# Optimization experiments

Hardware: AMD Instinct MI355X
Metric: run time of the kernel (lower is better)

Reference implementation:

```python
import jax, jax.numpy as jnp
import numpy as np

B, C, H_RES, W_RES = 8, 192, 64, 64


def dwconv(x, kern, pad):
    # depthwise conv, x: (B,C,H,W), kern: (C,1,k,k)
    return jax.lax.conv_general_dilated(
        x, kern, window_strides=(1, 1), padding=[(pad, pad), (pad, pad)],
        dimension_numbers=('NCHW', 'OIHW', 'NCHW'),
        feature_group_count=x.shape[1])


def omni_shift(x, alpha, dw1, dw3, dw5):
    # OmniShift (training branch): learnable mix of identity + depthwise 1x1/3x3/5x5
    return (alpha[0] * x + alpha[1] * dwconv(x, dw1, 0)
            + alpha[2] * dwconv(x, dw3, 1) + alpha[3] * dwconv(x, dw5, 2))


def biwkv(w, u, k, v):
    # Bidirectional WKV (Vision-RWKV style):
    # out_t = (sum_{i!=t} e^{-(|t-i|-1)w + k_i} v_i + e^{u+k_t} v_t)
    #       / (sum_{i!=t} e^{-(|t-i|-1)w + k_i}       + e^{u+k_t})
    # w,u: (C,); k,v: (B,T,C). Implemented as two stable log-scaled scans.
    kT = jnp.moveaxis(k, 1, 0)  # (T,B,C)
    vT = jnp.moveaxis(v, 1, 0)
    bc = (k.shape[0], k.shape[2])
    init = (jnp.full(bc, -jnp.inf, k.dtype), jnp.zeros(bc, k.dtype), jnp.zeros(bc, k.dtype))

    def step(carry, inp):
        p, num, den = carry          # state = e^p * (num, den) over strictly-previous tokens
        kt, vt = inp
        out = (p, num, den)          # emit BEFORE absorbing token t (i != t term)
        q = jnp.maximum(p - w, kt)
        e1 = jnp.exp(p - w - q)
        e2 = jnp.exp(kt - q)
        return (q, e1 * num + e2 * vt, e1 * den + e2), out

    _, (pf, nf, df) = jax.lax.scan(step, init, (kT, vT))
    _, (pb, nb, db) = jax.lax.scan(step, init, (kT[::-1], vT[::-1]))
    pb, nb, db = pb[::-1], nb[::-1], db[::-1]

    ps = u + kT                      # self term exponent
    r = jnp.maximum(jnp.maximum(pf, pb), ps)
    ef, eb, es = jnp.exp(pf - r), jnp.exp(pb - r), jnp.exp(ps - r)
    out = (ef * nf + eb * nb + es * vT) / (ef * df + eb * db + es)
    return jnp.moveaxis(out, 0, 1)   # (B,T,C)


def setup_inputs() -> dict:
    key = jax.random.key(0)
    ks = jax.random.split(key, 12)
    s = 1.0 / np.sqrt(C)
    inp = {
        'x': jax.random.normal(ks[0], (B, C, H_RES, W_RES), jnp.float32),
        'w_key': jax.random.normal(ks[1], (C, C), jnp.float32) * s,
        'w_value': jax.random.normal(ks[2], (C, C), jnp.float32) * s,
        'w_recept': jax.random.normal(ks[3], (C, C), jnp.float32) * s,
        'w_out': jax.random.normal(ks[4], (C, C), jnp.float32) * s,
        'decay': jax.random.normal(ks[5], (C,), jnp.float32),
        'boost': jax.random.normal(ks[6], (C,), jnp.float32),
        'alpha': jax.random.normal(ks[7], (4,), jnp.float32),
        'dw1': jax.random.normal(ks[8], (C, 1, 1, 1), jnp.float32) * s,
        'dw3': jax.random.normal(ks[9], (C, 1, 3, 3), jnp.float32) * (s / 3.0),
        'dw5': jax.random.normal(ks[10], (C, 1, 5, 5), jnp.float32) * (s / 5.0),
        'H': H_RES,
        'W': W_RES,
    }
    return inp


def reference(x, w_key, w_value, w_recept, w_out, decay, boost, alpha, dw1, dw3, dw5, H, W):
    Bn, Cn = x.shape[0], x.shape[1]
    T = H * W
    xs = omni_shift(x, alpha, dw1, dw3, dw5)                 # (B,C,H,W)
    xt = jnp.transpose(xs.reshape(Bn, Cn, T), (0, 2, 1))     # (B,T,C)
    k = jnp.einsum('btc,dc->btd', xt, w_key)
    v = jnp.einsum('btc,dc->btd', xt, w_value)
    sr = jax.nn.sigmoid(jnp.einsum('btc,dc->btd', xt, w_recept))
    y = biwkv(decay / T, boost / T, k, v)                    # (B,T,C)
    y = sr * y
    y = jnp.einsum('btd,cd->btc', y, w_out)
    return jnp.transpose(y, (0, 2, 1)).reshape(Bn, Cn, H, W)
```

## Files before the change

kernel.cpp:

```cpp
#include <hip/hip_runtime.h>
#include <math.h>

#define Cn 192
#define Bn 8
#define Tn 4096
#define HW 64

typedef unsigned short u16;
typedef unsigned int u32;
typedef __attribute__((ext_vector_type(8))) __bf16 bf16x8;
typedef __attribute__((ext_vector_type(16))) float f32x16;

__device__ __forceinline__ void gload16(const void* g, void* l) {
    __builtin_amdgcn_global_load_lds(
        (const __attribute__((address_space(1))) void*)g,
        (__attribute__((address_space(3))) void*)l, 16, 0, 0);
}

__device__ __forceinline__ void split_bf16(float x, u16 &h, u16 &l) {
    u32 u = __float_as_uint(x);
    u32 uh = (u + 0x7FFFu + ((u >> 16) & 1u)) & 0xFFFF0000u;
    h = (u16)(uh >> 16);
    float r = x - __uint_as_float(uh);
    u32 ur = __float_as_uint(r);
    l = (u16)((ur + 0x7FFFu + ((ur >> 16) & 1u)) >> 16);
}

__global__ __launch_bounds__(256) void omni_kernel(const float* __restrict__ x,
                                                   const float* __restrict__ alpha,
                                                   const float* __restrict__ dw1,
                                                   const float* __restrict__ dw3,
                                                   const float* __restrict__ dw5,
                                                   u16* __restrict__ xhi,
                                                   u16* __restrict__ xlo) {
    const int plane = blockIdx.x;
    const int c = plane % Cn;
    const float* xin = x + (size_t)plane * Tn;
    u16* oh = xhi + (size_t)plane * Tn;
    u16* ol = xlo + (size_t)plane * Tn;

    __shared__ float tile[68 * 68];
    __shared__ float wk[25];

    const int tid = threadIdx.x;
    if (tid == 0) {
        const float a0 = alpha[0], a1 = alpha[1], a2 = alpha[2], a3 = alpha[3];
        #pragma unroll
        for (int j = 0; j < 25; ++j) wk[j] = a3 * dw5[c * 25 + j];
        #pragma unroll
        for (int dy = 0; dy < 3; ++dy)
            #pragma unroll
            for (int dx = 0; dx < 3; ++dx)
                wk[(dy + 1) * 5 + (dx + 1)] += a2 * dw3[c * 9 + dy * 3 + dx];
        wk[12] += a1 * dw1[c] + a0;
    }
    for (int i = tid; i < 68 * 68; i += 256) {
        int r = i / 68, cc = i - r * 68;
        int gy = r - 2, gx = cc - 2;
        float v = 0.f;
        if (gy >= 0 && gy < HW && gx >= 0 && gx < HW) v = xin[gy * HW + gx];
        tile[i] = v;
    }
    __syncthreads();

    const int py = tid >> 3;
    const int px0 = (tid & 7) << 3;

    #pragma unroll
    for (int half = 0; half < 2; ++half) {
        const int y = py + half * 32;
        float row[5][12];
        #pragma unroll
        for (int dy = 0; dy < 5; ++dy) {
            const float4* rp = (const float4*)&tile[(y + dy) * 68 + px0];
            float4 r0 = rp[0], r1 = rp[1], r2 = rp[2];
            row[dy][0] = r0.x; row[dy][1] = r0.y; row[dy][2]  = r0.z; row[dy][3]  = r0.w;
            row[dy][4] = r1.x; row[dy][5] = r1.y; row[dy][6]  = r1.z; row[dy][7]  = r1.w;
            row[dy][8] = r2.x; row[dy][9] = r2.y; row[dy][10] = r2.z; row[dy][11] = r2.w;
        }
        u32 ph[4], pl[4];
        #pragma unroll
        for (int jj = 0; jj < 8; ++jj) {
            float acc = 0.f;
            #pragma unroll
            for (int dy = 0; dy < 5; ++dy)
                #pragma unroll
                for (int dx = 0; dx < 5; ++dx)
                    acc = fmaf(row[dy][jj + dx], wk[dy * 5 + dx], acc);
            u16 h, l2;
            split_bf16(acc, h, l2);
            if (jj & 1) { ph[jj >> 1] |= ((u32)h) << 16; pl[jj >> 1] |= ((u32)l2) << 16; }
            else        { ph[jj >> 1] = h;               pl[jj >> 1] = l2; }
        }
        *(uint4*)&oh[y * 64 + px0] = make_uint4(ph[0], ph[1], ph[2], ph[3]);
        *(uint4*)&ol[y * 64 + px0] = make_uint4(pl[0], pl[1], pl[2], pl[3]);
    }
}

__global__ __launch_bounds__(256) void transpose_kernel(const u16* __restrict__ ih,
                                                        const u16* __restrict__ il,
                                                        u16* __restrict__ oh,
                                                        u16* __restrict__ ol,
                                                        const float* __restrict__ Wk,
                                                        const float* __restrict__ Wv,
                                                        const float* __restrict__ Wr,
                                                        const float* __restrict__ Wo,
                                                        u16* __restrict__ wh,
                                                        u16* __restrict__ wl) {
    const int tid = threadIdx.x;
    if (blockIdx.z == 8) {
        const int base = (blockIdx.y * 32 + blockIdx.x) * 768;
        #pragma unroll
        for (int j = 0; j < 3; ++j) {
            int idx = base + j * 256 + tid;
            int mat = idx / 36864;
            int off = idx - mat * 36864;
            const float* src = (mat == 0) ? Wk : (mat == 1) ? Wv : (mat == 2) ? Wr : Wo;
            u16 h, l;
            split_bf16(src[off], h, l);
            wh[idx] = h;
            wl[idx] = l;
        }
        return;
    }

    __shared__ u32 T[2][128][21];
    const size_t ib = (size_t)blockIdx.z * Cn * Tn;
    const int c0 = blockIdx.y * 32, t0 = blockIdx.x * 128;

    {
        const int c2 = tid >> 4;
        const int tc = (tid & 15) * 8;
        const size_t ge = ib + (size_t)(c0 + 2 * c2) * Tn + t0 + tc;
        uint4 evh = *(const uint4*)&ih[ge];
        uint4 odh = *(const uint4*)&ih[ge + Tn];
        uint4 evl = *(const uint4*)&il[ge];
        uint4 odl = *(const uint4*)&il[ge + Tn];
        const u32 eh4[4] = {evh.x, evh.y, evh.z, evh.w};
        const u32 oh4[4] = {odh.x, odh.y, odh.z, odh.w};
        const u32 el4[4] = {evl.x, evl.y, evl.z, evl.w};
        const u32 ol4[4] = {odl.x, odl.y, odl.z, odl.w};
        #pragma unroll
        for (int q = 0; q < 4; ++q) {
            T[0][tc + 2 * q    ][c2] = (eh4[q] & 0xFFFFu) | (oh4[q] << 16);
            T[0][tc + 2 * q + 1][c2] = (eh4[q] >> 16) | (oh4[q] & 0xFFFF0000u);
            T[1][tc + 2 * q    ][c2] = (el4[q] & 0xFFFFu) | (ol4[q] << 16);
            T[1][tc + 2 * q + 1][c2] = (el4[q] >> 16) | (ol4[q] & 0xFFFF0000u);
        }
    }
    __syncthreads();
    {
        const int t = tid >> 1;
        const int hf = tid & 1;
        u32 wv[8][2];
        #pragma unroll
        for (int q = 0; q < 8; ++q) {
            wv[q][0] = T[0][t][hf * 8 + q];
            wv[q][1] = T[1][t][hf * 8 + q];
        }
        const size_t go = ib + (size_t)(t0 + t) * Cn + c0 + hf * 16;
        *(uint4*)&oh[go]     = make_uint4(wv[0][0], wv[1][0], wv[2][0], wv[3][0]);
        *(uint4*)&oh[go + 8] = make_uint4(wv[4][0], wv[5][0], wv[6][0], wv[7][0]);
        *(uint4*)&ol[go]     = make_uint4(wv[0][1], wv[1][1], wv[2][1], wv[3][1]);
        *(uint4*)&ol[go + 8] = make_uint4(wv[4][1], wv[5][1], wv[6][1], wv[7][1]);
    }
}

template<int NM>
__global__ __launch_bounds__(256) void gemm_mfma(const u16* __restrict__ wh,
                                                 const u16* __restrict__ wl,
                                                 const u16* __restrict__ Xh,
                                                 const u16* __restrict__ Xl,
                                                 float* __restrict__ O0,
                                                 float* __restrict__ O1,
                                                 float* __restrict__ O2,
                                                 int wrow0) {
    constexpr int ASZ = NM * 64 * 32;
    constexpr int BSZ = 128 * 32;
    __shared__ u16 A_[2 * ASZ];
    __shared__ u16 B_[2][2 * BSZ];

    const int tid  = threadIdx.x;
    const int l    = tid & 63;
    const int wave = tid >> 6;
    const int wm   = wave >> 1, wn = wave & 1;
    const int m0   = blockIdx.y * 64;
    const int t0   = blockIdx.x * 128;
    const size_t xb = (size_t)blockIdx.z * Cn * Tn;

    f32x16 acc[NM][2];
    #pragma unroll
    for (int m = 0; m < NM; ++m)
        #pragma unroll
        for (int nf = 0; nf < 2; ++nf)
            #pragma unroll
            for (int r = 0; r < 16; ++r) acc[m][nf][r] = 0.f;

    auto stageA = [&](int k0) {
        #pragma unroll
        for (int i = 0; i < NM; ++i) {
            int idx = i * 256 + tid;
            int row = idx >> 2;
            int cb  = (idx & 3) ^ ((row >> 1) & 3);
            int grow = wrow0 + (row >> 6) * 192 + m0 + (row & 63);
            int dst = (i * 256 + wave * 64) * 8;
            gload16(wh + (size_t)grow * Cn + k0 + cb * 8, A_ + dst);
            gload16(wl + (size_t)grow * Cn + k0 + cb * 8, A_ + ASZ + dst);
        }
    };
    auto stageB = [&](int bf, int k0) {
        #pragma unroll
        for (int i = 0; i < 2; ++i) {
            int idx = i * 256 + tid;
            int tr  = idx >> 2;
            int cb  = (idx & 3) ^ ((tr >> 1) & 3);
            int dst = (i * 256 + wave * 64) * 8;
            gload16(Xh + xb + (size_t)(t0 + tr) * Cn + k0 + cb * 8, B_[bf] + dst);
            gload16(Xl + xb + (size_t)(t0 + tr) * Cn + k0 + cb * 8, B_[bf] + BSZ + dst);
        }
    };
    auto compute = [&](int bf) {
        const u16* Ah = A_;
        const u16* Al = A_ + ASZ;
        const u16* Bh = B_[bf];
        const u16* Bl = B_[bf] + BSZ;
        #pragma unroll
        for (int kh = 0; kh < 2; ++kh) {
            const int cbb = kh * 2 + (l >> 5);
            bf16x8 ah[NM], al[NM];
            #pragma unroll
            for (int m = 0; m < NM; ++m) {
                int r = m * 64 + wm * 32 + (l & 31);
                int off = r * 32 + ((cbb ^ ((r >> 1) & 3)) << 3);
                ah[m] = *(const bf16x8*)&Ah[off];
                al[m] = *(const bf16x8*)&Al[off];
            }
            #pragma unroll
            for (int nf = 0; nf < 2; ++nf) {
                int tr = wn * 64 + nf * 32 + (l & 31);
                int off = tr * 32 + ((cbb ^ ((tr >> 1) & 3)) << 3);
                bf16x8 bh = *(const bf16x8*)&Bh[off];
                bf16x8 bl = *(const bf16x8*)&Bl[off];
                #pragma unroll
                for (int m = 0; m < NM; ++m) {
                    acc[m][nf] = __builtin_amdgcn_mfma_f32_32x32x16_bf16(ah[m], bh, acc[m][nf], 0, 0, 0);
                    acc[m][nf] = __builtin_amdgcn_mfma_f32_32x32x16_bf16(ah[m], bl, acc[m][nf], 0, 0, 0);
                    acc[m][nf] = __builtin_amdgcn_mfma_f32_32x32x16_bf16(al[m], bh, acc[m][nf], 0, 0, 0);
                }
            }
        }
    };

    stageA(0);
    stageB(0, 0);
    __syncthreads();
    for (int ks = 0; ks < 6; ++ks) {
        if (ks < 5) stageB((ks + 1) & 1, (ks + 1) * 32);
        compute(ks & 1);
        __syncthreads();
        if (ks < 5) {
            stageA((ks + 1) * 32);
            __syncthreads();
        }
    }

    float* Os[3] = {O0, O1, O2};
    #pragma unroll
    for (int m = 0; m < NM; ++m) {
        float* O = Os[m] + (size_t)blockIdx.z * Cn * Tn;
        #pragma unroll
        for (int nf = 0; nf < 2; ++nf) {
            int col = t0 + wn * 64 + nf * 32 + (l & 31);
            #pragma unroll
            for (int r = 0; r < 16; ++r) {
                int row = m0 + wm * 32 + (r & 3) + 8 * (r >> 2) + 4 * (l >> 5);
                O[(size_t)row * Tn + col] = acc[m][nf][r];
            }
        }
    }
}

__global__ __launch_bounds__(256) void wkv_kernel(const float* __restrict__ kg,
                                                  const float* __restrict__ vg,
                                                  const float* __restrict__ srlg,
                                                  const float* __restrict__ decay,
                                                  const float* __restrict__ boost,
                                                  u16* __restrict__ yhi,
                                                  u16* __restrict__ ylo) {
    const int row = blockIdx.x;
    const int d = row % Cn;
    const float* kr = kg + (size_t)row * Tn;
    const float* vr = vg + (size_t)row * Tn;
    const float* sr = srlg + (size_t)row * Tn;
    u16* yh = yhi + (size_t)row * Tn;
    u16* yl = ylo + (size_t)row * Tn;

    const int tid = threadIdx.x;
    const int t0 = tid * 16;

    float kk[16], vv[16];
    #pragma unroll
    for (int j = 0; j < 16; j += 4) {
        *(float4*)&kk[j] = *(const float4*)&kr[t0 + j];
        *(float4*)&vv[j] = *(const float4*)&vr[t0 + j];
    }

    __shared__ float red[256];
    float lm = kk[0];
    #pragma unroll
    for (int j = 1; j < 16; ++j) lm = fmaxf(lm, kk[j]);
    red[tid] = lm;
    __syncthreads();
    for (int s = 128; s > 0; s >>= 1) {
        if (tid < s) red[tid] = fmaxf(red[tid], red[tid + s]);
        __syncthreads();
    }
    const float m = red[0];
    __syncthreads();

    const float ww = decay[d] * (1.0f / (float)Tn);
    const float u = boost[d] * (1.0f / (float)Tn);
    const float lam = expf(-ww);
    const float lam16 = expf(-16.0f * ww);

    float a[16];
    #pragma unroll
    for (int j = 0; j < 16; ++j) a[j] = expf(kk[j] - m);

    float SN = 0.f, SD = 0.f;
    #pragma unroll
    for (int j = 0; j < 16; ++j) { SN = fmaf(lam, SN, a[j] * vv[j]); SD = fmaf(lam, SD, a[j]); }
    float BN = 0.f, BD = 0.f;
    #pragma unroll
    for (int j = 15; j >= 0; --j) { BN = fmaf(lam, BN, a[j] * vv[j]); BD = fmaf(lam, BD, a[j]); }

    __shared__ float sN[2][256], sD[2][256];

    sN[0][tid] = SN; sD[0][tid] = SD;
    __syncthreads();
    int src = 0;
    float f = lam16;
    for (int o = 1; o < 256; o <<= 1) {
        float nN = sN[src][tid], nD = sD[src][tid];
        if (tid >= o) { nN = fmaf(f, sN[src][tid - o], nN); nD = fmaf(f, sD[src][tid - o], nD); }
        sN[src ^ 1][tid] = nN; sD[src ^ 1][tid] = nD;
        __syncthreads();
        src ^= 1; f = f * f;
    }
    const float CfN = (tid > 0) ? sN[src][tid - 1] : 0.f;
    const float CfD = (tid > 0) ? sD[src][tid - 1] : 0.f;
    __syncthreads();

    sN[0][tid] = BN; sD[0][tid] = BD;
    __syncthreads();
    src = 0; f = lam16;
    for (int o = 1; o < 256; o <<= 1) {
        float nN = sN[src][tid], nD = sD[src][tid];
        if (tid + o < 256) { nN = fmaf(f, sN[src][tid + o], nN); nD = fmaf(f, sD[src][tid + o], nD); }
        sN[src ^ 1][tid] = nN; sD[src ^ 1][tid] = nD;
        __syncthreads();
        src ^= 1; f = f * f;
    }
    const float CbN = (tid < 255) ? sN[src][tid + 1] : 0.f;
    const float CbD = (tid < 255) ? sD[src][tid + 1] : 0.f;

    float fN[16], fD[16];
    float cN = CfN, cD = CfD;
    #pragma unroll
    for (int j = 0; j < 16; ++j) {
        fN[j] = cN; fD[j] = cD;
        cN = fmaf(lam, cN, a[j] * vv[j]);
        cD = fmaf(lam, cD, a[j]);
    }

    float sl[16];
    #pragma unroll
    for (int j = 0; j < 16; j += 4) *(float4*)&sl[j] = *(const float4*)&sr[t0 + j];

    u16 oh[16], ol[16];
    float bN = CbN, bD = CbD;
    #pragma unroll
    for (int j = 15; j >= 0; --j) {
        const float es = expf(u + kk[j] - m);
        const float num = fN[j] + bN + es * vv[j];
        const float den = fD[j] + bD + es;
        const float y = num / den;
        const float sig = 1.0f / (1.0f + expf(-sl[j]));
        split_bf16(sig * y, oh[j], ol[j]);
        bN = fmaf(lam, bN, a[j] * vv[j]);
        bD = fmaf(lam, bD, a[j]);
    }

    u32 ph[8], pl[8];
    #pragma unroll
    for (int j = 0; j < 8; ++j) {
        ph[j] = (u32)oh[2 * j] | ((u32)oh[2 * j + 1] << 16);
        pl[j] = (u32)ol[2 * j] | ((u32)ol[2 * j + 1] << 16);
    }
    *(uint4*)&yh[t0]     = make_uint4(ph[0], ph[1], ph[2], ph[3]);
    *(uint4*)&yh[t0 + 8] = make_uint4(ph[4], ph[5], ph[6], ph[7]);
    *(uint4*)&yl[t0]     = make_uint4(pl[0], pl[1], pl[2], pl[3]);
    *(uint4*)&yl[t0 + 8] = make_uint4(pl[4], pl[5], pl[6], pl[7]);
}

extern "C" void kernel_launch(void* const* d_in, const int* in_sizes, int n_in,
                              void* d_out, int out_size, void* d_ws, size_t ws_size,
                              hipStream_t stream) {
    const float* x        = (const float*)d_in[0];
    const float* w_key    = (const float*)d_in[1];
    const float* w_value  = (const float*)d_in[2];
    const float* w_recept = (const float*)d_in[3];
    const float* w_out    = (const float*)d_in[4];
    const float* decay    = (const float*)d_in[5];
    const float* boost    = (const float*)d_in[6];
    const float* alpha    = (const float*)d_in[7];
    const float* dw1      = (const float*)d_in[8];
    const float* dw3      = (const float*)d_in[9];
    const float* dw5      = (const float*)d_in[10];

    const size_t S = (size_t)Bn * Cn * Tn;
    u16* R0 = (u16*)d_ws;
    u16* R1 = R0 + 2 * S;
    u16* R2 = R1 + 2 * S;
    u16* whp = R2 + 2 * S;
    u16* wlp = whp + 4 * 36864;

    u16* xs_hi = R0;        u16* xs_lo = R0 + S;
    u16* Xt_hi = R1;        u16* Xt_lo = R1 + S;
    float* kb  = (float*)R0;
    float* vb  = (float*)R2;
    float* srl = (float*)d_out;
    u16* y_hi  = R1;        u16* y_lo  = R1 + S;
    u16* Yt_hi = R2;        u16* Yt_lo = R2 + S;
    float* out = (float*)d_out;

    omni_kernel<<<dim3(Bn * Cn), 256, 0, stream>>>(x, alpha, dw1, dw3, dw5, xs_hi, xs_lo);

    transpose_kernel<<<dim3(32, 6, 9), 256, 0, stream>>>(xs_hi, xs_lo, Xt_hi, Xt_lo,
                                                         w_key, w_value, w_recept, w_out,
                                                         whp, wlp);

    gemm_mfma<3><<<dim3(32, 3, 8), 256, 0, stream>>>(whp, wlp, Xt_hi, Xt_lo, kb, vb, srl, 0);

    wkv_kernel<<<dim3(Bn * Cn), 256, 0, stream>>>(kb, vb, srl, decay, boost, y_hi, y_lo);

    transpose_kernel<<<dim3(32, 6, 8), 256, 0, stream>>>(y_hi, y_lo, Yt_hi, Yt_lo,
                                                         w_key, w_value, w_recept, w_out,
                                                         whp, wlp);

    gemm_mfma<1><<<dim3(32, 3, 8), 256, 0, stream>>>(whp, wlp, Yt_hi, Yt_lo, out, nullptr, nullptr, 576);
}
```

Baseline: 119.2 us.

## Fuse transposes into GEMM B-loads and weight split into omni kernel

Removes both standalone transpose kernels. The GEMM now reads the channel-major bf16 hi/lo activations directly, transposes 4x4 u16 quads in registers with lane shuffles, and writes them into a padded, swizzled LDS buffer. A-operand weights are loaded straight from global memory into registers instead of being staged through LDS. The weight hi/lo split moves into extra blocks of the omni kernel, cutting two launches and the full activation round-trips through memory. In exchange it adds shuffle work and register pressure, plus a hand-managed barrier/prefetch pipeline with s_setprio.

Result: slower. 143.2 us (+20.2%).

```diff
diff --git a/kernel.cpp b/kernel.cpp
--- a/kernel.cpp
+++ b/kernel.cpp
@@ -10,12 +10,6 @@
 typedef unsigned int u32;
 typedef __attribute__((ext_vector_type(8))) __bf16 bf16x8;
 typedef __attribute__((ext_vector_type(16))) float f32x16;
-
-__device__ __forceinline__ void gload16(const void* g, void* l) {
-    __builtin_amdgcn_global_load_lds(
-        (const __attribute__((address_space(1))) void*)g,
-        (__attribute__((address_space(3))) void*)l, 16, 0, 0);
-}
 
 __device__ __forceinline__ void split_bf16(float x, u16 &h, u16 &l) {
     u32 u = __float_as_uint(x);
@@ -31,8 +25,31 @@
                                                    const float* __restrict__ dw1,
                                                    const float* __restrict__ dw3,
                                                    const float* __restrict__ dw5,
+                                                   const float* __restrict__ Wk,
+                                                   const float* __restrict__ Wv,
+                                                   const float* __restrict__ Wr,
+                                                   const float* __restrict__ Wo,
                                                    u16* __restrict__ xhi,
-                                                   u16* __restrict__ xlo) {
+                                                   u16* __restrict__ xlo,
+                                                   u16* __restrict__ wh,
+                                                   u16* __restrict__ wl) {
+    const int tid = threadIdx.x;
+    if (blockIdx.x >= 1536) {
+        const int base = (blockIdx.x - 1536) * 768;
+        #pragma unroll
+        for (int jj = 0; jj < 3; ++jj) {
+            int idx = base + jj * 256 + tid;
+            int mat = idx / 36864;
+            int off = idx - mat * 36864;
+            const float* src = (mat == 0) ? Wk : (mat == 1) ? Wv : (mat == 2) ? Wr : Wo;
+            u16 h, l;
+            split_bf16(src[off], h, l);
+            wh[idx] = h;
+            wl[idx] = l;
+        }
+        return;
+    }
+
     const int plane = blockIdx.x;
     const int c = plane % Cn;
     const float* xin = x + (size_t)plane * Tn;
@@ -42,7 +59,6 @@
     __shared__ float tile[68 * 68];
     __shared__ float wk[25];
 
-    const int tid = threadIdx.x;
     if (tid == 0) {
         const float a0 = alpha[0], a1 = alpha[1], a2 = alpha[2], a3 = alpha[3];
         #pragma unroll
@@ -97,88 +113,35 @@
     }
 }
 
-__global__ __launch_bounds__(256) void transpose_kernel(const u16* __restrict__ ih,
-                                                        const u16* __restrict__ il,
-                                                        u16* __restrict__ oh,
-                                                        u16* __restrict__ ol,
-                                                        const float* __restrict__ Wk,
-                                                        const float* __restrict__ Wv,
-                                                        const float* __restrict__ Wr,
-                                                        const float* __restrict__ Wo,
-                                                        u16* __restrict__ wh,
-                                                        u16* __restrict__ wl) {
-    const int tid = threadIdx.x;
-    if (blockIdx.z == 8) {
-        const int base = (blockIdx.y * 32 + blockIdx.x) * 768;
-        #pragma unroll
-        for (int j = 0; j < 3; ++j) {
-            int idx = base + j * 256 + tid;
-            int mat = idx / 36864;
-            int off = idx - mat * 36864;
-            const float* src = (mat == 0) ? Wk : (mat == 1) ? Wv : (mat == 2) ? Wr : Wo;
-            u16 h, l;
-            split_bf16(src[off], h, l);
-            wh[idx] = h;
-            wl[idx] = l;
-        }
-        return;
-    }
-
-    __shared__ u32 T[2][128][21];
-    const size_t ib = (size_t)blockIdx.z * Cn * Tn;
-    const int c0 = blockIdx.y * 32, t0 = blockIdx.x * 128;
-
-    {
-        const int c2 = tid >> 4;
-        const int tc = (tid & 15) * 8;
-        const size_t ge = ib + (size_t)(c0 + 2 * c2) * Tn + t0 + tc;
-        uint4 evh = *(const uint4*)&ih[ge];
-        uint4 odh = *(const uint4*)&ih[ge + Tn];
-        uint4 evl = *(const uint4*)&il[ge];
-        uint4 odl = *(const uint4*)&il[ge + Tn];
-        const u32 eh4[4] = {evh.x, evh.y, evh.z, evh.w};
-        const u32 oh4[4] = {odh.x, odh.y, odh.z, odh.w};
-        const u32 el4[4] = {evl.x, evl.y, evl.z, evl.w};
-        const u32 ol4[4] = {odl.x, odl.y, odl.z, odl.w};
-        #pragma unroll
-        for (int q = 0; q < 4; ++q) {
-            T[0][tc + 2 * q    ][c2] = (eh4[q] & 0xFFFFu) | (oh4[q] << 16);
-            T[0][tc + 2 * q + 1][c2] = (eh4[q] >> 16) | (oh4[q] & 0xFFFF0000u);
-            T[1][tc + 2 * q    ][c2] = (el4[q] & 0xFFFFu) | (ol4[q] << 16);
-            T[1][tc + 2 * q + 1][c2] = (el4[q] >> 16) | (ol4[q] & 0xFFFF0000u);
-        }
-    }
-    __syncthreads();
-    {
-        const int t = tid >> 1;
-        const int hf = tid & 1;
-        u32 wv[8][2];
-        #pragma unroll
-        for (int q = 0; q < 8; ++q) {
-            wv[q][0] = T[0][t][hf * 8 + q];
-            wv[q][1] = T[1][t][hf * 8 + q];
-        }
-        const size_t go = ib + (size_t)(t0 + t) * Cn + c0 + hf * 16;
-        *(uint4*)&oh[go]     = make_uint4(wv[0][0], wv[1][0], wv[2][0], wv[3][0]);
-        *(uint4*)&oh[go + 8] = make_uint4(wv[4][0], wv[5][0], wv[6][0], wv[7][0]);
-        *(uint4*)&ol[go]     = make_uint4(wv[0][1], wv[1][1], wv[2][1], wv[3][1]);
-        *(uint4*)&ol[go + 8] = make_uint4(wv[4][1], wv[5][1], wv[6][1], wv[7][1]);
-    }
+__device__ __forceinline__ uint2 quad_transpose(uint2 v, int j) {
+    unsigned int p0 = (unsigned int)__shfl_xor((int)v.x, 1);
+    unsigned int p1 = (unsigned int)__shfl_xor((int)v.y, 1);
+    unsigned int g0, g1;
+    if ((j & 1) == 0) {
+        g0 = (p0 << 16) | (v.x & 0xFFFFu);
+        g1 = (p1 << 16) | (v.y & 0xFFFFu);
+    } else {
+        g0 = (v.x & 0xFFFF0000u) | (p0 >> 16);
+        g1 = (v.y & 0xFFFF0000u) | (p1 >> 16);
+    }
+    unsigned int s0 = (unsigned int)__shfl_xor((int)g0, 2);
+    unsigned int s1 = (unsigned int)__shfl_xor((int)g1, 2);
+    uint2 f;
+    if ((j & 2) == 0) { f.x = g0; f.y = s0; }
+    else              { f.x = s1; f.y = g1; }
+    return f;
 }
 
 template<int NM>
-__global__ __launch_bounds__(256) void gemm_mfma(const u16* __restrict__ wh,
-                                                 const u16* __restrict__ wl,
-                                                 const u16* __restrict__ Xh,
-                                                 const u16* __restrict__ Xl,
-                                                 float* __restrict__ O0,
-                                                 float* __restrict__ O1,
-                                                 float* __restrict__ O2,
-                                                 int wrow0) {
-    constexpr int ASZ = NM * 64 * 32;
-    constexpr int BSZ = 128 * 32;
-    __shared__ u16 A_[2 * ASZ];
-    __shared__ u16 B_[2][2 * BSZ];
+__global__ __launch_bounds__(256) void gemm_fused(const u16* __restrict__ wh,
+                                                  const u16* __restrict__ wl,
+                                                  const u16* __restrict__ Xh,
+                                                  const u16* __restrict__ Xl,
+                                                  float* __restrict__ O0,
+                                                  float* __restrict__ O1,
+                                                  float* __restrict__ O2,
+                                                  int wrow0) {
+    __shared__ u16 B_[2][2][128 * 40];
 
     const int tid  = threadIdx.x;
     const int l    = tid & 63;
@@ -187,6 +150,7 @@
     const int m0   = blockIdx.y * 64;
     const int t0   = blockIdx.x * 128;
     const size_t xb = (size_t)blockIdx.z * Cn * Tn;
+    const int j    = tid & 3;
 
     f32x16 acc[NM][2];
     #pragma unroll
@@ -196,71 +160,89 @@
             #pragma unroll
             for (int r = 0; r < 16; ++r) acc[m][nf][r] = 0.f;
 
-    auto stageA = [&](int k0) {
-        #pragma unroll
-        for (int i = 0; i < NM; ++i) {
-            int idx = i * 256 + tid;
-            int row = idx >> 2;
-            int cb  = (idx & 3) ^ ((row >> 1) & 3);
-            int grow = wrow0 + (row >> 6) * 192 + m0 + (row & 63);
-            int dst = (i * 256 + wave * 64) * 8;
-            gload16(wh + (size_t)grow * Cn + k0 + cb * 8, A_ + dst);
-            gload16(wl + (size_t)grow * Cn + k0 + cb * 8, A_ + ASZ + dst);
+    uint2 rbh[4], rbl[4];
+    bf16x8 rah[NM][2], ral[NM][2];
+
+    auto loadB = [&](int k0) {
+        #pragma unroll
+        for (int p = 0; p < 4; ++p) {
+            int cq = 2 * p + (wave >> 1);
+            int tq = ((wave & 1) << 4) + (l >> 2);
+            size_t g = xb + (size_t)(k0 + cq * 4 + j) * Tn + t0 + tq * 4;
+            rbh[p] = *(const uint2*)&Xh[g];
+            rbl[p] = *(const uint2*)&Xl[g];
         }
     };
-    auto stageB = [&](int bf, int k0) {
-        #pragma unroll
-        for (int i = 0; i < 2; ++i) {
-            int idx = i * 256 + tid;
-            int tr  = idx >> 2;
-            int cb  = (idx & 3) ^ ((tr >> 1) & 3);
-            int dst = (i * 256 + wave * 64) * 8;
-            gload16(Xh + xb + (size_t)(t0 + tr) * Cn + k0 + cb * 8, B_[bf] + dst);
-            gload16(Xl + xb + (size_t)(t0 + tr) * Cn + k0 + cb * 8, B_[bf] + BSZ + dst);
-        }
+    auto writeB = [&](int bf) {
+        u16* Bh = &B_[bf][0][0];
+        u16* Bl = &B_[bf][1][0];
+        #pragma unroll
+        for (int p = 0; p < 4; ++p) {
+            int cq = 2 * p + (wave >> 1);
+            int tq = ((wave & 1) << 4) + (l >> 2);
+            uint2 th = quad_transpose(rbh[p], j);
+            uint2 tl = quad_transpose(rbl[p], j);
+            int t = tq * 4 + j;
+            int blk = ((cq >> 1) ^ (t >> 1) ^ (t >> 3)) & 3;
+            int off = t * 40 + (blk << 3) + ((cq & 1) << 2);
+            *(uint2*)&Bh[off] = th;
+            *(uint2*)&Bl[off] = tl;
+        }
+    };
+    auto loadA = [&](int k0) {
+        #pragma unroll
+        for (int m = 0; m < NM; ++m)
+            #pragma unroll
+            for (int kh = 0; kh < 2; ++kh) {
+                int cbb = kh * 2 + (l >> 5);
+                int r = wrow0 + m * 192 + m0 + wm * 32 + (l & 31);
+                size_t g = (size_t)r * Cn + k0 + cbb * 8;
+                rah[m][kh] = *(const bf16x8*)&wh[g];
+                ral[m][kh] = *(const bf16x8*)&wl[g];
+            }
     };
     auto compute = [&](int bf) {
-        const u16* Ah = A_;
-        const u16* Al = A_ + ASZ;
-        const u16* Bh = B_[bf];
-        const u16* Bl = B_[bf] + BSZ;
+        const u16* Bh = &B_[bf][0][0];
+        const u16* Bl = &B_[bf][1][0];
         #pragma unroll
         for (int kh = 0; kh < 2; ++kh) {
             const int cbb = kh * 2 + (l >> 5);
-            bf16x8 ah[NM], al[NM];
-            #pragma unroll
-            for (int m = 0; m < NM; ++m) {
-                int r = m * 64 + wm * 32 + (l & 31);
-                int off = r * 32 + ((cbb ^ ((r >> 1) & 3)) << 3);
-                ah[m] = *(const bf16x8*)&Ah[off];
-                al[m] = *(const bf16x8*)&Al[off];
-            }
             #pragma unroll
             for (int nf = 0; nf < 2; ++nf) {
-                int tr = wn * 64 + nf * 32 + (l & 31);
-                int off = tr * 32 + ((cbb ^ ((tr >> 1) & 3)) << 3);
+                int t = wn * 64 + nf * 32 + (l & 31);
+                int off = t * 40 + (((cbb ^ (t >> 1) ^ (t >> 3)) & 3) << 3);
                 bf16x8 bh = *(const bf16x8*)&Bh[off];
                 bf16x8 bl = *(const bf16x8*)&Bl[off];
                 #pragma unroll
                 for (int m = 0; m < NM; ++m) {
-                    acc[m][nf] = __builtin_amdgcn_mfma_f32_32x32x16_bf16(ah[m], bh, acc[m][nf], 0, 0, 0);
-                    acc[m][nf] = __builtin_amdgcn_mfma_f32_32x32x16_bf16(ah[m], bl, acc[m][nf], 0, 0, 0);
-                    acc[m][nf] = __builtin_amdgcn_mfma_f32_32x32x16_bf16(al[m], bh, acc[m][nf], 0, 0, 0);
+                    acc[m][nf] = __builtin_amdgcn_mfma_f32_32x32x16_bf16(rah[m][kh], bh, acc[m][nf], 0, 0, 0);
+                    acc[m][nf] = __builtin_amdgcn_mfma_f32_32x32x16_bf16(rah[m][kh], bl, acc[m][nf], 0, 0, 0);
+                    acc[m][nf] = __builtin_amdgcn_mfma_f32_32x32x16_bf16(ral[m][kh], bh, acc[m][nf], 0, 0, 0);
                 }
             }
         }
     };
 
-    stageA(0);
-    stageB(0, 0);
-    __syncthreads();
+    loadB(0);
+    loadA(0);
+    writeB(0);
+    loadB(32);
+    asm volatile("s_waitcnt lgkmcnt(0)" ::: "memory");
+    __builtin_amdgcn_sched_barrier(0);
+    __builtin_amdgcn_s_barrier();
+
+    #pragma unroll
     for (int ks = 0; ks < 6; ++ks) {
-        if (ks < 5) stageB((ks + 1) & 1, (ks + 1) * 32);
+        __builtin_amdgcn_s_setprio(1);
         compute(ks & 1);
-        __syncthreads();
+        __builtin_amdgcn_s_setprio(0);
         if (ks < 5) {
-            stageA((ks + 1) * 32);
-            __syncthreads();
+            writeB((ks + 1) & 1);
+            asm volatile("s_waitcnt lgkmcnt(0)" ::: "memory");
+            __builtin_amdgcn_sched_barrier(0);
+            __builtin_amdgcn_s_barrier();
+            if (ks < 4) loadB((ks + 2) * 32);
+            loadA((ks + 1) * 32);
         }
     }
 
@@ -426,27 +408,19 @@
     u16* wlp = whp + 4 * 36864;
 
     u16* xs_hi = R0;        u16* xs_lo = R0 + S;
-    u16* Xt_hi = R1;        u16* Xt_lo = R1 + S;
-    float* kb  = (float*)R0;
+    float* kb  = (float*)R1;
     float* vb  = (float*)R2;
     float* srl = (float*)d_out;
-    u16* y_hi  = R1;        u16* y_lo  = R1 + S;
-    u16* Yt_hi = R2;        u16* Yt_lo = R2 + S;
+    u16* y_hi  = R0;        u16* y_lo  = R0 + S;
     float* out = (float*)d_out;
 
-    omni_kernel<<<dim3(Bn * Cn), 256, 0, stream>>>(x, alpha, dw1, dw3, dw5, xs_hi, xs_lo);
-
-    transpose_kernel<<<dim3(32, 6, 9), 256, 0, stream>>>(xs_hi, xs_lo, Xt_hi, Xt_lo,
-                                                         w_key, w_value, w_recept, w_out,
-                                                         whp, wlp);
-
-    gemm_mfma<3><<<dim3(32, 3, 8), 256, 0, stream>>>(whp, wlp, Xt_hi, Xt_lo, kb, vb, srl, 0);
+    omni_kernel<<<dim3(1536 + 192), 256, 0, stream>>>(x, alpha, dw1, dw3, dw5,
+                                                      w_key, w_value, w_recept, w_out,
+                                                      xs_hi, xs_lo, whp, wlp);
+
+    gemm_fused<3><<<dim3(32, 3, 8), 256, 0, stream>>>(whp, wlp, xs_hi, xs_lo, kb, vb, srl, 0);
 
     wkv_kernel<<<dim3(Bn * Cn), 256, 0, stream>>>(kb, vb, srl, decay, boost, y_hi, y_lo);
 
-    transpose_kernel<<<dim3(32, 6, 8), 256, 0, stream>>>(y_hi, y_lo, Yt_hi, Yt_lo,
-                                                         w_key, w_value, w_recept, w_out,
-                                                         whp, wlp);
-
-    gemm_mfma<1><<<dim3(32, 3, 8), 256, 0, stream>>>(whp, wlp, Yt_hi, Yt_lo, out, nullptr, nullptr, 576);
-}
+    gemm_fused<1><<<dim3(32, 3, 8), 256, 0, stream>>>(whp, wlp, y_hi, y_lo, out, nullptr, nullptr, 576);
+}
```

## Single-buffer GEMM staging and move weight splitting into omni kernel

Applied to the files above, without the earlier changes.

Replaces the double-buffered B tile staging in the MFMA GEMM with a single shared buffer for A and B, loaded together with syncs on both sides of the load. This cuts LDS use per block, which may allow more resident blocks per CU, but load/compute overlap inside a block is lost. The fp32-to-bf16 hi/lo weight splitting moves from an extra z-slice of the first transpose launch into extra blocks of the omni convolution kernel, which simplifies the transpose kernel.

Measured after the change: 121.9 us. 1.02x slower.

```diff
diff --git a/kernel.cpp b/kernel.cpp
--- a/kernel.cpp
+++ b/kernel.cpp
@@ -31,8 +31,31 @@
                                                    const float* __restrict__ dw1,
                                                    const float* __restrict__ dw3,
                                                    const float* __restrict__ dw5,
+                                                   const float* __restrict__ Wk,
+                                                   const float* __restrict__ Wv,
+                                                   const float* __restrict__ Wr,
+                                                   const float* __restrict__ Wo,
                                                    u16* __restrict__ xhi,
-                                                   u16* __restrict__ xlo) {
+                                                   u16* __restrict__ xlo,
+                                                   u16* __restrict__ wh,
+                                                   u16* __restrict__ wl) {
+    const int tid = threadIdx.x;
+    if (blockIdx.x >= 1536) {
+        const int base = (blockIdx.x - 1536) * 768;
+        #pragma unroll
+        for (int jj = 0; jj < 3; ++jj) {
+            int idx = base + jj * 256 + tid;
+            int mat = idx / 36864;
+            int off = idx - mat * 36864;
+            const float* src = (mat == 0) ? Wk : (mat == 1) ? Wv : (mat == 2) ? Wr : Wo;
+            u16 h, l;
+            split_bf16(src[off], h, l);
+            wh[idx] = h;
+            wl[idx] = l;
+        }
+        return;
+    }
+
     const int plane = blockIdx.x;
     const int c = plane % Cn;
     const float* xin = x + (size_t)plane * Tn;
@@ -42,7 +65,6 @@
     __shared__ float tile[68 * 68];
     __shared__ float wk[25];
 
-    const int tid = threadIdx.x;
     if (tid == 0) {
         const float a0 = alpha[0], a1 = alpha[1], a2 = alpha[2], a3 = alpha[3];
         #pragma unroll
@@ -100,31 +122,9 @@
 __global__ __launch_bounds__(256) void transpose_kernel(const u16* __restrict__ ih,
                                                         const u16* __restrict__ il,
                                                         u16* __restrict__ oh,
-                                                        u16* __restrict__ ol,
-                                                        const float* __restrict__ Wk,
-                                                        const float* __restrict__ Wv,
-                                                        const float* __restrict__ Wr,
-                                                        const float* __restrict__ Wo,
-                                                        u16* __restrict__ wh,
-                                                        u16* __restrict__ wl) {
+                                                        u16* __restrict__ ol) {
+    __shared__ u32 T[2][128][21];
     const int tid = threadIdx.x;
-    if (blockIdx.z == 8) {
-        const int base = (blockIdx.y * 32 + blockIdx.x) * 768;
-        #pragma unroll
-        for (int j = 0; j < 3; ++j) {
-            int idx = base + j * 256 + tid;
-            int mat = idx / 36864;
-            int off = idx - mat * 36864;
-            const float* src = (mat == 0) ? Wk : (mat == 1) ? Wv : (mat == 2) ? Wr : Wo;
-            u16 h, l;
-            split_bf16(src[off], h, l);
-            wh[idx] = h;
-            wl[idx] = l;
-        }
-        return;
-    }
-
-    __shared__ u32 T[2][128][21];
     const size_t ib = (size_t)blockIdx.z * Cn * Tn;
     const int c0 = blockIdx.y * 32, t0 = blockIdx.x * 128;
 
@@ -177,8 +177,8 @@
                                                  int wrow0) {
     constexpr int ASZ = NM * 64 * 32;
     constexpr int BSZ = 128 * 32;
-    __shared__ u16 A_[2 * ASZ];
-    __shared__ u16 B_[2][2 * BSZ];
+    __shared__ u16 Ah_[ASZ], Al_[ASZ];
+    __shared__ u16 Bh_[BSZ], Bl_[BSZ];
 
     const int tid  = threadIdx.x;
     const int l    = tid & 63;
@@ -196,7 +196,7 @@
             #pragma unroll
             for (int r = 0; r < 16; ++r) acc[m][nf][r] = 0.f;
 
-    auto stageA = [&](int k0) {
+    auto stage = [&](int k0) {
         #pragma unroll
         for (int i = 0; i < NM; ++i) {
             int idx = i * 256 + tid;
@@ -204,26 +204,21 @@
             int cb  = (idx & 3) ^ ((row >> 1) & 3);
             int grow = wrow0 + (row >> 6) * 192 + m0 + (row & 63);
             int dst = (i * 256 + wave * 64) * 8;
-            gload16(wh + (size_t)grow * Cn + k0 + cb * 8, A_ + dst);
-            gload16(wl + (size_t)grow * Cn + k0 + cb * 8, A_ + ASZ + dst);
-        }
-    };
-    auto stageB = [&](int bf, int k0) {
+            gload16(wh + (size_t)grow * Cn + k0 + cb * 8, Ah_ + dst);
+            gload16(wl + (size_t)grow * Cn + k0 + cb * 8, Al_ + dst);
+        }
         #pragma unroll
         for (int i = 0; i < 2; ++i) {
             int idx = i * 256 + tid;
             int tr  = idx >> 2;
             int cb  = (idx & 3) ^ ((tr >> 1) & 3);
             int dst = (i * 256 + wave * 64) * 8;
-            gload16(Xh + xb + (size_t)(t0 + tr) * Cn + k0 + cb * 8, B_[bf] + dst);
-            gload16(Xl + xb + (size_t)(t0 + tr) * Cn + k0 + cb * 8, B_[bf] + BSZ + dst);
+            gload16(Xh + xb + (size_t)(t0 + tr) * Cn + k0 + cb * 8, Bh_ + dst);
+            gload16(Xl + xb + (size_t)(t0 + tr) * Cn + k0 + cb * 8, Bl_ + dst);
         }
     };
-    auto compute = [&](int bf) {
-        const u16* Ah = A_;
-        const u16* Al = A_ + ASZ;
-        const u16* Bh = B_[bf];
-        const u16* Bl = B_[bf] + BSZ;
+
+    auto compute = [&]() {
         #pragma unroll
         for (int kh = 0; kh < 2; ++kh) {
             const int cbb = kh * 2 + (l >> 5);
@@ -232,15 +227,15 @@
             for (int m = 0; m < NM; ++m) {
                 int r = m * 64 + wm * 32 + (l & 31);
                 int off = r * 32 + ((cbb ^ ((r >> 1) & 3)) << 3);
-                ah[m] = *(const bf16x8*)&Ah[off];
-                al[m] = *(const bf16x8*)&Al[off];
+                ah[m] = *(const bf16x8*)&Ah_[off];
+                al[m] = *(const bf16x8*)&Al_[off];
             }
             #pragma unroll
             for (int nf = 0; nf < 2; ++nf) {
                 int tr = wn * 64 + nf * 32 + (l & 31);
                 int off = tr * 32 + ((cbb ^ ((tr >> 1) & 3)) << 3);
-                bf16x8 bh = *(const bf16x8*)&Bh[off];
-                bf16x8 bl = *(const bf16x8*)&Bl[off];
+                bf16x8 bh = *(const bf16x8*)&Bh_[off];
+                bf16x8 bl = *(const bf16x8*)&Bl_[off];
                 #pragma unroll
                 for (int m = 0; m < NM; ++m) {
                     acc[m][nf] = __builtin_amdgcn_mfma_f32_32x32x16_bf16(ah[m], bh, acc[m][nf], 0, 0, 0);
@@ -251,15 +246,13 @@
         }
     };
 
-    stageA(0);
-    stageB(0, 0);
+    stage(0);
     __syncthreads();
     for (int ks = 0; ks < 6; ++ks) {
-        if (ks < 5) stageB((ks + 1) & 1, (ks + 1) * 32);
-        compute(ks & 1);
-        __syncthreads();
+        compute();
         if (ks < 5) {
-            stageA((ks + 1) * 32);
+            __syncthreads();
+            stage((ks + 1) * 32);
             __syncthreads();
         }
     }
@@ -434,19 +427,17 @@
     u16* Yt_hi = R2;        u16* Yt_lo = R2 + S;
     float* out = (float*)d_out;
 
-    omni_kernel<<<dim3(Bn * Cn), 256, 0, stream>>>(x, alpha, dw1, dw3, dw5, xs_hi, xs_lo);
-
-    transpose_kernel<<<dim3(32, 6, 9), 256, 0, stream>>>(xs_hi, xs_lo, Xt_hi, Xt_lo,
-                                                         w_key, w_value, w_recept, w_out,
-                                                         whp, wlp);
+    omni_kernel<<<dim3(1536 + 192), 256, 0, stream>>>(x, alpha, dw1, dw3, dw5,
+                                                      w_key, w_value, w_recept, w_out,
+                                                      xs_hi, xs_lo, whp, wlp);
+
+    transpose_kernel<<<dim3(32, 6, 8), 256, 0, stream>>>(xs_hi, xs_lo, Xt_hi, Xt_lo);
 
     gemm_mfma<3><<<dim3(32, 3, 8), 256, 0, stream>>>(whp, wlp, Xt_hi, Xt_lo, kb, vb, srl, 0);
 
     wkv_kernel<<<dim3(Bn * Cn), 256, 0, stream>>>(kb, vb, srl, decay, boost, y_hi, y_lo);
 
-    transpose_kernel<<<dim3(32, 6, 8), 256, 0, stream>>>(y_hi, y_lo, Yt_hi, Yt_lo,
-                                                         w_key, w_value, w_recept, w_out,
-                                                         whp, wlp);
+    transpose_kernel<<<dim3(32, 6, 8), 256, 0, stream>>>(y_hi, y_lo, Yt_hi, Yt_lo);
 
     gemm_mfma<1><<<dim3(32, 3, 8), 256, 0, stream>>>(whp, wlp, Yt_hi, Yt_lo, out, nullptr, nullptr, 576);
 }
```
